# Kernel tuning notes

Measured on AMD Instinct MI355X. Metric: run time of the kernel, lower is better.

Reference implementation:

```python
import jax, jax.numpy as jnp
import numpy as np

N = 8192
D_IN, D_H, D_OUT = 512, 256, 128
BETA = 0.8
EPS = 1e-08


def _xavier(key, fan_in, fan_out):
    limit = float(np.sqrt(6.0 / (fan_in + fan_out)))
    return jax.random.uniform(key, (fan_in, fan_out), jnp.float32, -limit, limit)


def setup_inputs() -> dict:
    key = jax.random.key(0)
    kA, kS, kx, kw1, kw2 = jax.random.split(key, 5)
    A = jax.random.uniform(kA, (N, N), jnp.float32)
    S = jax.random.uniform(kS, (N, N), jnp.float32)
    x = jax.random.normal(kx, (N, D_IN), jnp.float32)
    W1 = _xavier(kw1, D_IN, D_H)
    b1 = jnp.zeros((D_H,), jnp.float32)
    W2 = _xavier(kw2, D_H, D_OUT)
    b2 = jnp.zeros((D_OUT,), jnp.float32)
    return {"A": A, "S": S, "x": x, "W1": W1, "b1": b1, "W2": W2, "b2": b2}


def _normalize_adj(adj):
    # adj + eps * I  (add only on the diagonal; no dense eye materialized)
    idx = jnp.arange(adj.shape[0])
    adj = adj.at[idx, idx].add(EPS)
    d = adj.sum(axis=1)                       # [N]
    d_inv_sqrt = d ** -0.5
    d_inv_sqrt = jnp.where(jnp.isinf(d_inv_sqrt), 0.0, d_inv_sqrt)
    # D^{-1/2} A D^{-1/2} as broadcast row/col scaling (same math as diag matmuls)
    return d_inv_sqrt[:, None] * adj * d_inv_sqrt[None, :]


def reference(A, S, x, W1, b1, W2, b2):
    A_tilde = A + BETA * S                    # [N, N]
    A_norm = _normalize_adj(A_tilde)          # [N, N]
    # GCN layer 1: relu(A_norm @ (x @ W1) + b1)   (dropout is identity at eval)
    h = jax.nn.relu(A_norm @ (x @ W1) + b1)   # [N, D_H]
    # GCN layer 2 (output layer, no activation)
    out = A_norm @ (h @ W2) + b2              # [N, D_OUT]
    return out
```

## Files before the change

### kernel.cpp

```cpp
#include <hip/hip_runtime.h>

#define EPS 1e-8f
#define BETA 0.8f

typedef __attribute__((ext_vector_type(8))) short bf16x8;
typedef __attribute__((ext_vector_type(4))) float f32x4;
typedef __attribute__((ext_vector_type(4))) float float4v;
typedef __attribute__((ext_vector_type(4))) unsigned short ushort4v;

__device__ __forceinline__ unsigned short f2b(float f) {
  unsigned int u = __builtin_bit_cast(unsigned int, f);
  u += 0x7fffu + ((u >> 16) & 1u);
  return (unsigned short)(u >> 16);
}

__global__ __launch_bounds__(256) void k_degree_convert(
    const float* __restrict__ A, const float* __restrict__ S,
    unsigned short* __restrict__ At, float* __restrict__ dis) {
  const int row = blockIdx.x;
  const int tid = threadIdx.x;
  const size_t base = (size_t)row * 8192;
  float4v a[8], s[8];
#pragma unroll
  for (int i = 0; i < 8; ++i) {
    const int c = i * 1024 + tid * 4;
    a[i] = __builtin_nontemporal_load(
        reinterpret_cast<const float4v*>(A + base + c));
    s[i] = __builtin_nontemporal_load(
        reinterpret_cast<const float4v*>(S + base + c));
  }
  float sum = 0.f;
#pragma unroll
  for (int i = 0; i < 8; ++i) {
    const int c = i * 1024 + tid * 4;
    float v0 = a[i].x + BETA * s[i].x;
    float v1 = a[i].y + BETA * s[i].y;
    float v2 = a[i].z + BETA * s[i].z;
    float v3 = a[i].w + BETA * s[i].w;
    sum += (v0 + v1) + (v2 + v3);
    ushort4v o = {f2b(v0), f2b(v1), f2b(v2), f2b(v3)};
    *reinterpret_cast<ushort4v*>(At + base + c) = o;
  }
#pragma unroll
  for (int off = 32; off > 0; off >>= 1) sum += __shfl_xor(sum, off, 64);
  __shared__ float wsum[4];
  if ((tid & 63) == 0) wsum[tid >> 6] = sum;
  __syncthreads();
  if (tid == 0) {
    float d = ((wsum[0] + wsum[1]) + (wsum[2] + wsum[3])) + EPS;
    dis[row] = (d > 0.f) ? 1.0f / sqrtf(d) : 0.f;
  }
}

__global__ __launch_bounds__(256) void k_conv_bf16(
    const float* __restrict__ in, unsigned short* __restrict__ out, int n4) {
  int idx = blockIdx.x * 256 + threadIdx.x;
  if (idx >= n4) return;
  float4v v = reinterpret_cast<const float4v*>(in)[idx];
  ushort4v o = {f2b(v.x), f2b(v.y), f2b(v.z), f2b(v.w)};
  reinterpret_cast<ushort4v*>(out)[idx] = o;
}

__global__ __launch_bounds__(256) void k_convT(
    const float* __restrict__ W, unsigned short* __restrict__ WT, int R, int C) {
  int idx = blockIdx.x * 256 + threadIdx.x;
  if (idx >= R * C) return;
  int r = idx / C, c = idx - r * C;
  WT[c * R + r] = f2b(W[idx]);
}

template <int BM, int BN, int EPI>
__global__ __launch_bounds__(256) void k_gemm_bt(
    const unsigned short* __restrict__ Ag, const unsigned short* __restrict__ BTg,
    int M, int N, int Kstride, int Kchunk,
    const float* __restrict__ dis, const float* __restrict__ bias,
    float* __restrict__ outf, unsigned short* __restrict__ outb) {
  constexpr int WM = BM / 2, WN = BN / 2;
  constexpr int MF = WM / 16, NF = WN / 16;
  constexpr int NLOADS = BM / 32 + BN / 32;
  __shared__ unsigned short Als[2][BM][64];
  __shared__ unsigned short Bls[2][BN][64];
  const int tid = threadIdx.x;
  const int lane = tid & 63;
  const int wm = (tid >> 6) >> 1, wn = (tid >> 6) & 1;
  const int brow = blockIdx.x * BM, bcol = blockIdx.y * BN;
  const int ar = tid >> 3;
  const int ac = (tid & 7) * 8;
  const int l15 = lane & 15, lk = (lane >> 4) * 8;

  f32x4 acc[MF][NF];
#pragma unroll
  for (int i = 0; i < MF; ++i)
#pragma unroll
    for (int j = 0; j < NF; ++j) acc[i][j] = (f32x4){0.f, 0.f, 0.f, 0.f};

  auto stage = [&](int buf, int k0) {
#pragma unroll
    for (int i = 0; i < BM / 32; ++i) {
      const unsigned short* g =
          Ag + (size_t)(brow + i * 32 + ar) * Kstride + k0 + ac;
      __builtin_amdgcn_global_load_lds(
          (const __attribute__((address_space(1))) void*)g,
          (__attribute__((address_space(3))) void*)&Als[buf][i * 32 + ar][ac],
          16, 0, 0);
    }
#pragma unroll
    for (int i = 0; i < BN / 32; ++i) {
      const unsigned short* g =
          BTg + (size_t)(bcol + i * 32 + ar) * Kstride + k0 + ac;
      __builtin_amdgcn_global_load_lds(
          (const __attribute__((address_space(1))) void*)g,
          (__attribute__((address_space(3))) void*)&Bls[buf][i * 32 + ar][ac],
          16, 0, 0);
    }
  };

  const int nsteps = Kchunk / 64;
  stage(0, 0);
  for (int t = 0; t < nsteps; ++t) {
    const int cur = t & 1;
    if (t + 1 < nsteps) {
      stage(cur ^ 1, (t + 1) * 64);
      asm volatile("s_waitcnt vmcnt(%0)" ::"n"(NLOADS));
    } else {
      asm volatile("s_waitcnt vmcnt(0)");
    }
    __builtin_amdgcn_s_barrier();
    asm volatile("" ::: "memory");
#pragma unroll
    for (int kk = 0; kk < 2; ++kk) {
      bf16x8 afr[MF], bfr[NF];
#pragma unroll
      for (int mi = 0; mi < MF; ++mi)
        afr[mi] = *reinterpret_cast<const bf16x8*>(
            &Als[cur][wm * WM + mi * 16 + l15][kk * 32 + lk]);
#pragma unroll
      for (int ni = 0; ni < NF; ++ni)
        bfr[ni] = *reinterpret_cast<const bf16x8*>(
            &Bls[cur][wn * WN + ni * 16 + l15][kk * 32 + lk]);
#pragma unroll
      for (int mi = 0; mi < MF; ++mi)
#pragma unroll
        for (int ni = 0; ni < NF; ++ni)
          acc[mi][ni] = __builtin_amdgcn_mfma_f32_16x16x32_bf16(
              afr[mi], bfr[ni], acc[mi][ni], 0, 0, 0);
    }
    asm volatile("" ::: "memory");
    __builtin_amdgcn_s_barrier();
  }

  const int crow0 = brow + wm * WM, ccol0 = bcol + wn * WN;
#pragma unroll
  for (int mi = 0; mi < MF; ++mi) {
    const int row0 = crow0 + mi * 16 + (lane >> 4) * 4;
    const float d0 = dis[row0], d1 = dis[row0 + 1], d2 = dis[row0 + 2],
                d3 = dis[row0 + 3];
#pragma unroll
    for (int ni = 0; ni < NF; ++ni) {
      const int col = ccol0 + ni * 16 + l15;
      f32x4 a = acc[mi][ni];
      if constexpr (EPI == 0) {
        ushort4v o = {f2b(d0 * a.x), f2b(d1 * a.y), f2b(d2 * a.z),
                      f2b(d3 * a.w)};
        *reinterpret_cast<ushort4v*>(outb + (size_t)col * M + row0) = o;
      } else if constexpr (EPI == 1) {
        const float bb = bias[col];
        float v0 = d0 * a.x + bb; v0 = v0 > 0.f ? v0 : 0.f;
        float v1 = d1 * a.y + bb; v1 = v1 > 0.f ? v1 : 0.f;
        float v2 = d2 * a.z + bb; v2 = v2 > 0.f ? v2 : 0.f;
        float v3 = d3 * a.w + bb; v3 = v3 > 0.f ? v3 : 0.f;
        outb[(size_t)(row0 + 0) * N + col] = f2b(v0);
        outb[(size_t)(row0 + 1) * N + col] = f2b(v1);
        outb[(size_t)(row0 + 2) * N + col] = f2b(v2);
        outb[(size_t)(row0 + 3) * N + col] = f2b(v3);
      } else {
        const float bb = bias[col];
        outf[(size_t)(row0 + 0) * N + col] = d0 * a.x + bb;
        outf[(size_t)(row0 + 1) * N + col] = d1 * a.y + bb;
        outf[(size_t)(row0 + 2) * N + col] = d2 * a.z + bb;
        outf[(size_t)(row0 + 3) * N + col] = d3 * a.w + bb;
      }
    }
  }
}

template <int BM, int BN, int WGM, int WGN>
__global__ __launch_bounds__(512, 2) void k_gemm_split(
    const unsigned short* __restrict__ Ag,
    const unsigned short* __restrict__ BTg,
    int M, int N, int Kstride, int Kchunk, int gx,
    float* __restrict__ P) {
  constexpr int NLOADS = BM / 64 + BN / 64;
  __shared__ unsigned short Als[2][BM][64];
  __shared__ unsigned short Bls[2][BN][64];

  const int nblk = gridDim.x;
  const int flat = blockIdx.x;
  const int cpx = nblk >> 3;
  const int swz = (flat & 7) * cpx + (flat >> 3);
  const int bx = swz % gx;
  const int bz = swz / gx;

  const int tid = threadIdx.x;
  const int lane = tid & 63;
  const int wid = tid >> 6;
  const int wm = wid / WGN, wn = wid % WGN;
  const int brow = bx * BM;
  const int kbase = bz * Kchunk;
  const int ar = tid >> 3;
  const int ac = (tid & 7) * 8;
  const int l15 = lane & 15, lk = (lane >> 4) * 8;

  f32x4 acc[4][4];
#pragma unroll
  for (int i = 0; i < 4; ++i)
#pragma unroll
    for (int j = 0; j < 4; ++j) acc[i][j] = (f32x4){0.f, 0.f, 0.f, 0.f};

  auto stage = [&](int buf, int k0) {
#pragma unroll
    for (int i = 0; i < BM / 64; ++i) {
      const unsigned short* g =
          Ag + (size_t)(brow + i * 64 + ar) * Kstride + k0 + ac;
      __builtin_amdgcn_global_load_lds(
          (const __attribute__((address_space(1))) void*)g,
          (__attribute__((address_space(3))) void*)&Als[buf][i * 64 + ar][ac],
          16, 0, 0);
    }
#pragma unroll
    for (int i = 0; i < BN / 64; ++i) {
      const unsigned short* g = BTg + (size_t)(i * 64 + ar) * Kstride + k0 + ac;
      __builtin_amdgcn_global_load_lds(
          (const __attribute__((address_space(1))) void*)g,
          (__attribute__((address_space(3))) void*)&Bls[buf][i * 64 + ar][ac],
          16, 0, 0);
    }
  };

  const int nsteps = Kchunk / 64;
  stage(0, kbase);
  for (int t = 0; t < nsteps; ++t) {
    const int cur = t & 1;
    if (t + 1 < nsteps) {
      stage(cur ^ 1, kbase + (t + 1) * 64);
      asm volatile("s_waitcnt vmcnt(%0)" ::"n"(NLOADS));
    } else {
      asm volatile("s_waitcnt vmcnt(0)");
    }
    __builtin_amdgcn_s_barrier();
    asm volatile("" ::: "memory");
#pragma unroll
    for (int kk = 0; kk < 2; ++kk) {
      bf16x8 afr[4], bfr[4];
#pragma unroll
      for (int mi = 0; mi < 4; ++mi)
        afr[mi] = *reinterpret_cast<const bf16x8*>(
            &Als[cur][wm * 64 + mi * 16 + l15][kk * 32 + lk]);
#pragma unroll
      for (int ni = 0; ni < 4; ++ni)
        bfr[ni] = *reinterpret_cast<const bf16x8*>(
            &Bls[cur][wn * 64 + ni * 16 + l15][kk * 32 + lk]);
#pragma unroll
      for (int mi = 0; mi < 4; ++mi)
#pragma unroll
        for (int ni = 0; ni < 4; ++ni)
          acc[mi][ni] = __builtin_amdgcn_mfma_f32_16x16x32_bf16(
              afr[mi], bfr[ni], acc[mi][ni], 0, 0, 0);
    }
    asm volatile("" ::: "memory");
    __builtin_amdgcn_s_barrier();
  }

  float* Pz = P + (size_t)bz * M * N;
  const int crow0 = brow + wm * 64, ccol0 = wn * 64;
#pragma unroll
  for (int mi = 0; mi < 4; ++mi) {
    const int row0 = crow0 + mi * 16 + (lane >> 4) * 4;
#pragma unroll
    for (int ni = 0; ni < 4; ++ni) {
      const int col = ccol0 + ni * 16 + l15;
      f32x4 a = acc[mi][ni];
      Pz[(size_t)(row0 + 0) * N + col] = a.x;
      Pz[(size_t)(row0 + 1) * N + col] = a.y;
      Pz[(size_t)(row0 + 2) * N + col] = a.z;
      Pz[(size_t)(row0 + 3) * N + col] = a.w;
    }
  }
}

template <int MODE, int NS>
__global__ __launch_bounds__(256) void k_reduceN(
    const float* __restrict__ P, int M, int N,
    const float* __restrict__ dis, const float* __restrict__ bias,
    unsigned short* __restrict__ outb, float* __restrict__ outf) {
  const int idx = blockIdx.x * 256 + threadIdx.x;
  const int row = idx / (N / 4);
  const int c0 = (idx - row * (N / 4)) * 4;
  const size_t off = (size_t)row * N + c0;
  const size_t ps = (size_t)M * N;
  float r0 = 0.f, r1 = 0.f, r2 = 0.f, r3 = 0.f;
#pragma unroll
  for (int z = 0; z < NS; ++z) {
    float4v v = *reinterpret_cast<const float4v*>(P + z * ps + off);
    r0 += v.x; r1 += v.y; r2 += v.z; r3 += v.w;
  }
  const float d = dis[row];
  float4v bb = *reinterpret_cast<const float4v*>(bias + c0);
  r0 = d * r0 + bb.x; r1 = d * r1 + bb.y;
  r2 = d * r2 + bb.z; r3 = d * r3 + bb.w;
  if constexpr (MODE == 0) {
    r0 = r0 > 0.f ? r0 : 0.f;
    r1 = r1 > 0.f ? r1 : 0.f;
    r2 = r2 > 0.f ? r2 : 0.f;
    r3 = r3 > 0.f ? r3 : 0.f;
    ushort4v o = {f2b(r0), f2b(r1), f2b(r2), f2b(r3)};
    *reinterpret_cast<ushort4v*>(outb + off) = o;
  } else {
    float4v o = {r0, r1, r2, r3};
    *reinterpret_cast<float4v*>(outf + off) = o;
  }
}

extern "C" void kernel_launch(void* const* d_in, const int* in_sizes, int n_in,
                              void* d_out, int out_size, void* d_ws,
                              size_t ws_size, hipStream_t stream) {
  const float* A  = (const float*)d_in[0];
  const float* S  = (const float*)d_in[1];
  const float* x  = (const float*)d_in[2];
  const float* W1 = (const float*)d_in[3];
  const float* b1 = (const float*)d_in[4];
  const float* W2 = (const float*)d_in[5];
  const float* b2 = (const float*)d_in[6];
  float* out = (float*)d_out;

  char* ws = (char*)d_ws;
  dim3 blk(256);

  const size_t O_At = 0, O_xb = 134217728, O_M1T = 142606336,
               O_P = 146800640, O_W1T = 180355072, O_W2T = 180617216,
               O_dis = 180682752, NEED = 180715520;

  if (ws_size >= NEED) {
    unsigned short* At  = (unsigned short*)(ws + O_At);
    unsigned short* xb  = (unsigned short*)(ws + O_xb);
    unsigned short* M1T = (unsigned short*)(ws + O_M1T);
    float*          P   = (float*)(ws + O_P);
    unsigned short* hb  = (unsigned short*)(ws + O_M1T);
    unsigned short* M2T = (unsigned short*)(ws + O_xb);
    unsigned short* W1T = (unsigned short*)(ws + O_W1T);
    unsigned short* W2T = (unsigned short*)(ws + O_W2T);
    float*          dis = (float*)(ws + O_dis);

    k_degree_convert<<<8192, blk, 0, stream>>>(A, S, At, dis);
    k_conv_bf16<<<4096, blk, 0, stream>>>(x, xb, 4194304 / 4);
    k_convT<<<512, blk, 0, stream>>>(W1, W1T, 512, 256);
    k_convT<<<128, blk, 0, stream>>>(W2, W2T, 256, 128);
    k_gemm_bt<128, 64, 0><<<dim3(64, 4), blk, 0, stream>>>(
        xb, W1T, 8192, 256, 512, 512, dis, nullptr, nullptr, M1T);
    k_gemm_split<128, 256, 2, 4><<<dim3(256), dim3(512), 0, stream>>>(
        At, M1T, 8192, 256, 8192, 2048, 64, P);
    k_reduceN<0, 4><<<2048, blk, 0, stream>>>(P, 8192, 256, dis, b1, hb,
                                              nullptr);
    k_gemm_bt<64, 64, 0><<<dim3(128, 2), blk, 0, stream>>>(
        hb, W2T, 8192, 128, 256, 256, dis, nullptr, nullptr, M2T);
    k_gemm_split<256, 128, 4, 2><<<dim3(256), dim3(512), 0, stream>>>(
        At, M2T, 8192, 128, 8192, 1024, 32, P);
    k_reduceN<1, 8><<<1024, blk, 0, stream>>>(P, 8192, 128, dis, b2, nullptr,
                                              out);
  } else {
    unsigned short* At  = (unsigned short*)(ws);
    unsigned short* xb  = (unsigned short*)(ws + 134217728);
    unsigned short* M1T = (unsigned short*)(ws + 142606336);
    unsigned short* hb  = (unsigned short*)(ws + 146800640);
    unsigned short* M2T = (unsigned short*)(ws + 150994944);
    unsigned short* W1T = (unsigned short*)(ws + 153092096);
    unsigned short* W2T = (unsigned short*)(ws + 153354240);
    float* dis          = (float*)(ws + 153419776);

    k_degree_convert<<<8192, blk, 0, stream>>>(A, S, At, dis);
    k_conv_bf16<<<4096, blk, 0, stream>>>(x, xb, 4194304 / 4);
    k_convT<<<512, blk, 0, stream>>>(W1, W1T, 512, 256);
    k_convT<<<128, blk, 0, stream>>>(W2, W2T, 256, 128);
    k_gemm_bt<128, 64, 0><<<dim3(64, 4), blk, 0, stream>>>(
        xb, W1T, 8192, 256, 512, 512, dis, nullptr, nullptr, M1T);
    k_gemm_bt<128, 64, 1><<<dim3(64, 4), blk, 0, stream>>>(
        At, M1T, 8192, 256, 8192, 8192, dis, b1, nullptr, hb);
    k_gemm_bt<64, 64, 0><<<dim3(128, 2), blk, 0, stream>>>(
        hb, W2T, 8192, 128, 256, 256, dis, nullptr, nullptr, M2T);
    k_gemm_bt<64, 64, 2><<<dim3(128, 2), blk, 0, stream>>>(
        At, M2T, 8192, 128, 8192, 8192, dis, b2, out, nullptr);
  }
}
```

Baseline: 236.9 us.

## Triple-buffer split GEMM LDS pipeline and merge conversion kernels into one launch

```diff
diff --git a/kernel.cpp b/kernel.cpp
--- a/kernel.cpp
+++ b/kernel.cpp
@@ -52,21 +52,25 @@
   }
 }
 
-__global__ __launch_bounds__(256) void k_conv_bf16(
-    const float* __restrict__ in, unsigned short* __restrict__ out, int n4) {
-  int idx = blockIdx.x * 256 + threadIdx.x;
-  if (idx >= n4) return;
-  float4v v = reinterpret_cast<const float4v*>(in)[idx];
-  ushort4v o = {f2b(v.x), f2b(v.y), f2b(v.z), f2b(v.w)};
-  reinterpret_cast<ushort4v*>(out)[idx] = o;
-}
-
-__global__ __launch_bounds__(256) void k_convT(
-    const float* __restrict__ W, unsigned short* __restrict__ WT, int R, int C) {
-  int idx = blockIdx.x * 256 + threadIdx.x;
-  if (idx >= R * C) return;
-  int r = idx / C, c = idx - r * C;
-  WT[c * R + r] = f2b(W[idx]);
+__global__ __launch_bounds__(256) void k_conv_all(
+    const float* __restrict__ x, unsigned short* __restrict__ xb,
+    const float* __restrict__ W1, unsigned short* __restrict__ W1T,
+    const float* __restrict__ W2, unsigned short* __restrict__ W2T) {
+  const int b = blockIdx.x;
+  if (b < 4096) {
+    const int idx = b * 256 + threadIdx.x;
+    float4v v = reinterpret_cast<const float4v*>(x)[idx];
+    ushort4v o = {f2b(v.x), f2b(v.y), f2b(v.z), f2b(v.w)};
+    reinterpret_cast<ushort4v*>(xb)[idx] = o;
+  } else if (b < 4608) {
+    const int idx = (b - 4096) * 256 + threadIdx.x;
+    const int r = idx >> 8, c = idx & 255;
+    W1T[c * 512 + r] = f2b(W1[idx]);
+  } else {
+    const int idx = (b - 4608) * 256 + threadIdx.x;
+    const int r = idx >> 7, c = idx & 127;
+    W2T[c * 256 + r] = f2b(W2[idx]);
+  }
 }
 
 template <int BM, int BN, int EPI>
@@ -191,8 +195,8 @@
     int M, int N, int Kstride, int Kchunk, int gx,
     float* __restrict__ P) {
   constexpr int NLOADS = BM / 64 + BN / 64;
-  __shared__ unsigned short Als[2][BM][64];
-  __shared__ unsigned short Bls[2][BN][64];
+  __shared__ unsigned short Als[3][BM][64];
+  __shared__ unsigned short Bls[3][BN][64];
 
   const int nblk = gridDim.x;
   const int flat = blockIdx.x;
@@ -239,10 +243,13 @@
 
   const int nsteps = Kchunk / 64;
   stage(0, kbase);
+  stage(1, kbase + 64);
   for (int t = 0; t < nsteps; ++t) {
-    const int cur = t & 1;
-    if (t + 1 < nsteps) {
-      stage(cur ^ 1, kbase + (t + 1) * 64);
+    const int cur = t % 3;
+    if (t + 2 < nsteps) {
+      stage((t + 2) % 3, kbase + (t + 2) * 64);
+      asm volatile("s_waitcnt vmcnt(%0)" ::"n"(2 * NLOADS));
+    } else if (t + 1 < nsteps) {
       asm volatile("s_waitcnt vmcnt(%0)" ::"n"(NLOADS));
     } else {
       asm volatile("s_waitcnt vmcnt(0)");
@@ -352,9 +359,7 @@
     float*          dis = (float*)(ws + O_dis);
 
     k_degree_convert<<<8192, blk, 0, stream>>>(A, S, At, dis);
-    k_conv_bf16<<<4096, blk, 0, stream>>>(x, xb, 4194304 / 4);
-    k_convT<<<512, blk, 0, stream>>>(W1, W1T, 512, 256);
-    k_convT<<<128, blk, 0, stream>>>(W2, W2T, 256, 128);
+    k_conv_all<<<4736, blk, 0, stream>>>(x, xb, W1, W1T, W2, W2T);
     k_gemm_bt<128, 64, 0><<<dim3(64, 4), blk, 0, stream>>>(
         xb, W1T, 8192, 256, 512, 512, dis, nullptr, nullptr, M1T);
     k_gemm_split<128, 256, 2, 4><<<dim3(256), dim3(512), 0, stream>>>(
@@ -378,9 +383,7 @@
     float* dis          = (float*)(ws + 153419776);
 
     k_degree_convert<<<8192, blk, 0, stream>>>(A, S, At, dis);
-    k_conv_bf16<<<4096, blk, 0, stream>>>(x, xb, 4194304 / 4);
-    k_convT<<<512, blk, 0, stream>>>(W1, W1T, 512, 256);
-    k_convT<<<128, blk, 0, stream>>>(W2, W2T, 256, 128);
+    k_conv_all<<<4736, blk, 0, stream>>>(x, xb, W1, W1T, W2, W2T);
     k_gemm_bt<128, 64, 0><<<dim3(64, 4), blk, 0, stream>>>(
         xb, W1T, 8192, 256, 512, 512, dis, nullptr, nullptr, M1T);
     k_gemm_bt<128, 64, 1><<<dim3(64, 4), blk, 0, stream>>>(
```

Result: no change. 234.3 us (-1.1%).
